# Kernel optimization log

Measured on AMD Instinct MI355X. Metric: run time of the kernel, lower is better.

## Reference

```python
import jax, jax.numpy as jnp
import numpy as np
from jax.scipy.special import logsumexp

S, B, T = 512, 1024, 48


def setup_inputs() -> dict:
    key = jax.random.key(0)
    k1, k2, k3, k4, k5 = jax.random.split(key, 5)
    return {
        "emissions": jax.random.normal(k1, (S, B, T), jnp.float32),
        "tags": jax.random.randint(k2, (S, B), 0, T, jnp.int32),
        "mask": jnp.ones((S, B), jnp.float32),
        "transitions": jax.random.normal(k3, (T, T), jnp.float32),
        "start_transitions": jax.random.normal(k4, (T,), jnp.float32),
        "stop_transitions": jax.random.normal(k5, (T,), jnp.float32),
    }


def _crf(emissions, tags, mask, transitions, start, stop):
    # emissions: (S,B,T), tags/mask: (S,B), time-major as in the torch module
    init = start[None, :] + emissions[0]  # (B,T)

    def step(carry, inp):
        fv, vv = carry  # forward (logsumexp) and viterbi (max) vars, each (B,T)
        em, m = inp  # (B,T), (B,)
        # scores[b, next, prev] = prev_var + transitions[prev,next] swapped to match
        # torch: forward_var.unsqueeze(1) + emission.unsqueeze(2) + transitions.unsqueeze(0)
        sc_f = fv[:, None, :] + transitions[None, :, :] + em[:, :, None]  # (B,T,T)
        sc_v = vv[:, None, :] + transitions[None, :, :] + em[:, :, None]
        new_fv = logsumexp(sc_f, axis=2)
        new_vv = jnp.max(sc_v, axis=2)
        m_ = m[:, None]
        fv = m_ * new_fv + (1.0 - m_) * fv
        vv = m_ * new_vv + (1.0 - m_) * vv
        return (fv, vv), None

    (fv, vv), _ = jax.lax.scan(step, (init, init), (emissions[1:], mask[1:]))
    alpha = logsumexp(fv + stop[None, :], axis=1)  # total_score (B,)
    best_path_score = jnp.max(vv + stop[None, :], axis=1)  # (B,)

    # real (gold) path score, fully vectorized over time
    em_tag = jnp.take_along_axis(emissions, tags[:, :, None].astype(jnp.int32), axis=2)[:, :, 0]  # (S,B)
    trans_sc = transitions[tags[:-1], tags[1:]]  # (S-1,B)
    real = (start[tags[0]]
            + jnp.sum(mask[1:] * (trans_sc + em_tag[1:]), axis=0)
            + stop[tags[-1]])
    loss = jnp.mean(alpha - real)
    return loss, real, alpha, best_path_score


def reference(emissions, tags, mask, transitions, start_transitions, stop_transitions):
    # Training-mode forward (return_best_path=False -> best_path is None in torch)
    return _crf(emissions, tags, mask, transitions, start_transitions, stop_transitions)
```

## Files before the change

kernel.cpp:

```cpp
#include <hip/hip_runtime.h>
#include <hip/hip_fp16.h>

#define S_LEN 512
#define B_DIM 1024
#define T_DIM 48
#define L2E 1.4426950408889634f
#define LN2 0.6931471805599453f

#define EXP2F(x) __builtin_amdgcn_exp2f(x)
#define LOG2F(x) __builtin_amdgcn_logf(x)

typedef _Float16 h2v __attribute__((ext_vector_type(2)));

__device__ __forceinline__ __half2 hmax2(__half2 a, __half2 b) {
  h2v r = __builtin_elementwise_max(__builtin_bit_cast(h2v, a),
                                    __builtin_bit_cast(h2v, b));
  return __builtin_bit_cast(__half2, r);
}

__device__ __forceinline__ __half2 bpick(__half2 src, int lane) {
  int s = __builtin_amdgcn_readlane(__builtin_bit_cast(int, src), lane);
  return __builtin_bit_cast(__half2, s);
}

template <int CTRL, int RMASK>
__device__ __forceinline__ float dppmovf(float v) {
  return __int_as_float(__builtin_amdgcn_update_dpp(
      __float_as_int(v), __float_as_int(v), CTRL, RMASK, 0xF, false));
}
template <int CTRL, int RMASK>
__device__ __forceinline__ float dppmaxf(float m) {
  return fmaxf(m, dppmovf<CTRL, RMASK>(m));
}
template <int CTRL, int RMASK>
__device__ __forceinline__ float dppaddf(float m) {
  return m + dppmovf<CTRL, RMASK>(m);
}

__device__ __forceinline__ float wave_max63(float m) {
  m = dppmaxf<0xB1, 0xF>(m);
  m = dppmaxf<0x4E, 0xF>(m);
  m = dppmaxf<0x141, 0xF>(m);
  m = dppmaxf<0x140, 0xF>(m);
  m = dppmaxf<0x142, 0xA>(m);
  m = dppmaxf<0x143, 0xC>(m);
  return __int_as_float(__builtin_amdgcn_readlane(__float_as_int(m), 63));
}
__device__ __forceinline__ float wave_sum63(float m) {
  m = dppaddf<0xB1, 0xF>(m);
  m = dppaddf<0x4E, 0xF>(m);
  m = dppaddf<0x141, 0xF>(m);
  m = dppaddf<0x140, 0xF>(m);
  m = dppaddf<0x142, 0xA>(m);
  m = dppaddf<0x143, 0xC>(m);
  return __int_as_float(__builtin_amdgcn_readlane(__float_as_int(m), 63));
}

__global__ __launch_bounds__(192, 3)
void crf_fused(const float* __restrict__ em, const int* __restrict__ tags,
               const float* __restrict__ mask, const float* __restrict__ trans,
               const float* __restrict__ startT, const float* __restrict__ stopT,
               float* __restrict__ out)
{
  const int b    = blockIdx.x;
  const int wave = threadIdx.x >> 6;
  const int i    = threadIdx.x & 63;

  if (wave == 2) {
    float acc = 0.f;
#pragma unroll
    for (int k = 0; k < 8; ++k) {
      int s = 1 + i + (k << 6);
      if (s < S_LEN) {
        int   tp  = tags[(s - 1) * B_DIM + b];
        int   tc  = tags[s * B_DIM + b];
        float mkv = mask[s * B_DIM + b];
        float emt = em[((size_t)s * B_DIM + b) * T_DIM + tc];
        acc = fmaf(mkv, trans[tp * T_DIM + tc] + emt, acc);
      }
    }
    float tot = wave_sum63(acc);
    if (i == 0)
      out[1 + b] = startT[tags[b]] + stopT[tags[(S_LEN - 1) * B_DIM + b]] + tot;
    return;
  }

  const int ri = (i < T_DIM) ? i : (T_DIM - 1);

  const float* emb = em + (size_t)b * T_DIM + ri;
  const size_t estep = (size_t)B_DIM * T_DIM;
  float e1 = emb[1 * estep], e2 = emb[2 * estep], e3 = emb[3 * estep];
  float e4 = emb[4 * estep], e5 = emb[5 * estep], e6 = emb[6 * estep];
  float mk1 = mask[1 * B_DIM + b], mk2 = mask[2 * B_DIM + b];
  float mk3 = mask[3 * B_DIM + b], mk4 = mask[4 * B_DIM + b];
  float mk5 = mask[5 * B_DIM + b], mk6 = mask[6 * B_DIM + b];
  const float* pf  = emb + 7 * estep;
  const float* pmk = mask + 7 * B_DIM + b;

#define SHIFT_REGS                                                   \
      e1 = e2; e2 = e3; e3 = e4; e4 = e5; e5 = e6; e6 = ep;          \
      mk1 = mk2; mk2 = mk3; mk3 = mk4; mk4 = mk5; mk5 = mk6; mk6 = mkp;

  if (wave == 0) {
#define DECL_E(n) __half2 E##n = __floats2half2_rn( \
      EXP2F(trans[ri * T_DIM + 2*(n)    ] * L2E),   \
      EXP2F(trans[ri * T_DIM + 2*(n) + 1] * L2E));
    DECL_E(0)  DECL_E(1)  DECL_E(2)  DECL_E(3)  DECL_E(4)  DECL_E(5)
    DECL_E(6)  DECL_E(7)  DECL_E(8)  DECL_E(9)  DECL_E(10) DECL_E(11)
    DECL_E(12) DECL_E(13) DECL_E(14) DECL_E(15) DECL_E(16) DECL_E(17)
    DECL_E(18) DECL_E(19) DECL_E(20) DECL_E(21) DECL_E(22) DECL_E(23)

#define PIN_E asm("" : "+v"(E0), "+v"(E1), "+v"(E2), "+v"(E3),       \
      "+v"(E4), "+v"(E5), "+v"(E6), "+v"(E7), "+v"(E8), "+v"(E9),    \
      "+v"(E10), "+v"(E11), "+v"(E12), "+v"(E13), "+v"(E14),         \
      "+v"(E15), "+v"(E16), "+v"(E17), "+v"(E18), "+v"(E19),         \
      "+v"(E20), "+v"(E21), "+v"(E22), "+v"(E23));

    float p  = EXP2F((startT[ri] + emb[0]) * L2E);
    float k2 = 0.f;

#define FVG(g, Ea, Eb, Ec, Ed, Ee, Ef)                 \
    { __half2 t0 = bpick(pp, 12*(g) + 0);              \
      __half2 t1 = bpick(pp, 12*(g) + 2);              \
      __half2 t2 = bpick(pp, 12*(g) + 4);              \
      __half2 t3 = bpick(pp, 12*(g) + 6);              \
      __half2 t4 = bpick(pp, 12*(g) + 8);              \
      __half2 t5 = bpick(pp, 12*(g) + 10);             \
      a0 = __hfma2(t0, Ea, a0);                        \
      a1 = __hfma2(t1, Eb, a1);                        \
      a2 = __hfma2(t2, Ec, a2);                        \
      a3 = __hfma2(t3, Ed, a3);                        \
      a0 = __hfma2(t4, Ee, a0);                        \
      a1 = __hfma2(t5, Ef, a1); }

#define FV_STEP(LOAD)                                                \
    { float ep, mkp;                                                 \
      if (LOAD) { ep = *pf; pf += estep; mkp = *pmk; pmk += B_DIM; } \
      else      { ep = e6; mkp = mk6; }                              \
      PIN_E                                                          \
      float pm = wave_max63(p);               \
      float lg = LOG2F(pm);                                          \
      float c  = EXP2F(-lg - 8.0f);                   \
      k2 += lg + 8.0f;                                               \
      float pn = dppmovf<0xB1, 0xF>(p);                              \
      __half2 pp = __floats2half2_rn(p, pn);                         \
      __half2 a0 = __float2half2_rn(0.f), a1 = a0, a2 = a0, a3 = a0; \
      FVG(0, E0,  E1,  E2,  E3,  E4,  E5)                            \
      FVG(1, E6,  E7,  E8,  E9,  E10, E11)                           \
      FVG(2, E12, E13, E14, E15, E16, E17)                           \
      FVG(3, E18, E19, E20, E21, E22, E23)                           \
      a0 = __hadd2(a0, a1); a2 = __hadd2(a2, a3); a0 = __hadd2(a0, a2); \
      float accF  = __low2float(a0) + __high2float(a0);              \
      float expem = EXP2F(e1 * L2E);                                 \
      float t  = accF * expem * c;                                   \
      float pc = p * c;                                              \
      p = fminf(fmaf(mk1, t - pc, pc), 1024.0f);                     \
      SHIFT_REGS }

#pragma unroll 6
    for (int s = 1; s <= 504; ++s) FV_STEP(true)
    FV_STEP(true)
    FV_STEP(false) FV_STEP(false) FV_STEP(false)
    FV_STEP(false) FV_STEP(false) FV_STEP(false)

    float q = p * EXP2F(stopT[ri] * L2E);
    q = (i < T_DIM) ? q : 0.f;
    float Sq = wave_sum63(q);
    float alpha = LN2 * (k2 + LOG2F(Sq));
    if (i == 0) out[1 + B_DIM + b] = alpha;
  } else {
#define DECL_T(n) __half2 T##n = __floats2half2_rn( \
      trans[ri * T_DIM + 2*(n)], trans[ri * T_DIM + 2*(n) + 1]);
    DECL_T(0)  DECL_T(1)  DECL_T(2)  DECL_T(3)  DECL_T(4)  DECL_T(5)
    DECL_T(6)  DECL_T(7)  DECL_T(8)  DECL_T(9)  DECL_T(10) DECL_T(11)
    DECL_T(12) DECL_T(13) DECL_T(14) DECL_T(15) DECL_T(16) DECL_T(17)
    DECL_T(18) DECL_T(19) DECL_T(20) DECL_T(21) DECL_T(22) DECL_T(23)

#define PIN_T asm("" : "+v"(T0), "+v"(T1), "+v"(T2), "+v"(T3),       \
      "+v"(T4), "+v"(T5), "+v"(T6), "+v"(T7), "+v"(T8), "+v"(T9),    \
      "+v"(T10), "+v"(T11), "+v"(T12), "+v"(T13), "+v"(T14),         \
      "+v"(T15), "+v"(T16), "+v"(T17), "+v"(T18), "+v"(T19),         \
      "+v"(T20), "+v"(T21), "+v"(T22), "+v"(T23));

    float v = startT[ri] + emb[0];
    const __half2 NEGI = __floats2half2_rn(-60000.f, -60000.f);
    float m_ref = wave_max63(v);

#define VVG(g, Ta, Tb, Tc, Td, Te, Tf)                 \
    { __half2 t0 = bpick(vp, 12*(g) + 0);              \
      __half2 t1 = bpick(vp, 12*(g) + 2);              \
      __half2 t2 = bpick(vp, 12*(g) + 4);              \
      __half2 t3 = bpick(vp, 12*(g) + 6);              \
      __half2 t4 = bpick(vp, 12*(g) + 8);              \
      __half2 t5 = bpick(vp, 12*(g) + 10);             \
      m0 = hmax2(m0, __hadd2(t0, Ta));                 \
      m1 = hmax2(m1, __hadd2(t1, Tb));                 \
      m2 = hmax2(m2, __hadd2(t2, Tc));                 \
      m3 = hmax2(m3, __hadd2(t3, Td));                 \
      m0 = hmax2(m0, __hadd2(t4, Te));                 \
      m1 = hmax2(m1, __hadd2(t5, Tf)); }

#define VV_STEP(LOAD, DOTREE)                                        \
    { float ep, mkp;                                                 \
      if (LOAD) { ep = *pf; pf += estep; mkp = *pmk; pmk += B_DIM; } \
      else      { ep = e6; mkp = mk6; }                              \
      PIN_T                                                          \
      if (DOTREE) m_ref = wave_max63(v);                             \
      float vr  = v - m_ref;                                         \
      float vn_ = dppmovf<0xB1, 0xF>(vr);                            \
      __half2 vp = __floats2half2_rn(vr, vn_);                       \
      __half2 m0 = NEGI, m1 = NEGI, m2 = NEGI, m3 = NEGI;            \
      VVG(0, T0,  T1,  T2,  T3,  T4,  T5)                            \
      VVG(1, T6,  T7,  T8,  T9,  T10, T11)                           \
      VVG(2, T12, T13, T14, T15, T16, T17)                           \
      VVG(3, T18, T19, T20, T21, T22, T23)                           \
      m0 = hmax2(hmax2(m0, m1), hmax2(m2, m3));                      \
      float mx = fmaxf(__low2float(m0), __high2float(m0));           \
      float vnew = e1 + m_ref + mx;                                  \
      v = fmaf(mk1, vnew - v, v);                                    \
      SHIFT_REGS }

#pragma unroll 8
    for (int s = 1; s <= 504; ++s) VV_STEP(true, ((s & 7) == 0))
    VV_STEP(true, false)
    VV_STEP(false, false) VV_STEP(false, false) VV_STEP(false, false)
    VV_STEP(false, false) VV_STEP(false, false) VV_STEP(false, false)

    float best = wave_max63(v + stopT[ri]);
    if (i == 0) out[1 + 2 * B_DIM + b] = best;
  }
}

__global__ __launch_bounds__(256)
void crf_loss(float* __restrict__ out)
{
  __shared__ float red[256];
  int t = threadIdx.x;
  float a = 0.f;
  for (int b = t; b < B_DIM; b += 256)
    a += out[1 + B_DIM + b] - out[1 + b];
  red[t] = a;
  __syncthreads();
  for (int w = 128; w > 0; w >>= 1) {
    if (t < w) red[t] += red[t + w];
    __syncthreads();
  }
  if (t == 0) out[0] = red[0] * (1.0f / B_DIM);
}

extern "C" void kernel_launch(void* const* d_in, const int* in_sizes, int n_in,
                              void* d_out, int out_size, void* d_ws, size_t ws_size,
                              hipStream_t stream) {
  (void)in_sizes; (void)n_in; (void)d_ws; (void)ws_size; (void)out_size;
  const float* em     = (const float*)d_in[0];
  const int*   tags   = (const int*)d_in[1];
  const float* mask   = (const float*)d_in[2];
  const float* trans  = (const float*)d_in[3];
  const float* startT = (const float*)d_in[4];
  const float* stopT  = (const float*)d_in[5];
  float* out = (float*)d_out;

  hipLaunchKernelGGL(crf_fused, dim3(B_DIM), dim3(192), 0, stream,
                     em, tags, mask, trans, startT, stopT, out);
  hipLaunchKernelGGL(crf_loss, dim3(1), dim3(256), 0, stream, out);
}
```

Before: 201.5 us.

## Lockstep waves with periodic barriers and replace log/exp rescale with exponent bit tricks

Restructures the forward and Viterbi time loops into 63 groups of 8 steps, with a workgroup barrier after each group. The gold-path wave joins the same barriers, so the three waves stay in lockstep and their loads and issue slots may interleave better. The per-step log2/exp2 rescale in the forward wave is replaced by reading the float exponent bits and building a power-of-two scale factor. The per-step register pin asm becomes a single volatile pin before each loop. Barriers add stall points if the waves run at different speeds, and dropping the per-step pin may let the compiler spill or reload the transition registers.

```diff
diff --git a/kernel.cpp b/kernel.cpp
--- a/kernel.cpp
+++ b/kernel.cpp
@@ -68,16 +68,18 @@
 
   if (wave == 2) {
     float acc = 0.f;
-#pragma unroll
-    for (int k = 0; k < 8; ++k) {
-      int s = 1 + i + (k << 6);
-      if (s < S_LEN) {
-        int   tp  = tags[(s - 1) * B_DIM + b];
-        int   tc  = tags[s * B_DIM + b];
-        float mkv = mask[s * B_DIM + b];
-        float emt = em[((size_t)s * B_DIM + b) * T_DIM + tc];
-        acc = fmaf(mkv, trans[tp * T_DIM + tc] + emt, acc);
+    for (int g = 0; g < 63; ++g) {
+      if (g < 8) {
+        int s = 1 + i + (g << 6);
+        if (s < S_LEN) {
+          int   tp  = tags[(s - 1) * B_DIM + b];
+          int   tc  = tags[s * B_DIM + b];
+          float mkv = mask[s * B_DIM + b];
+          float emt = em[((size_t)s * B_DIM + b) * T_DIM + tc];
+          acc = fmaf(mkv, trans[tp * T_DIM + tc] + emt, acc);
+        }
       }
+      __builtin_amdgcn_s_barrier();
     }
     float tot = wave_sum63(acc);
     if (i == 0)
@@ -110,10 +112,10 @@
     DECL_E(12) DECL_E(13) DECL_E(14) DECL_E(15) DECL_E(16) DECL_E(17)
     DECL_E(18) DECL_E(19) DECL_E(20) DECL_E(21) DECL_E(22) DECL_E(23)
 
-#define PIN_E asm("" : "+v"(E0), "+v"(E1), "+v"(E2), "+v"(E3),       \
-      "+v"(E4), "+v"(E5), "+v"(E6), "+v"(E7), "+v"(E8), "+v"(E9),    \
-      "+v"(E10), "+v"(E11), "+v"(E12), "+v"(E13), "+v"(E14),         \
-      "+v"(E15), "+v"(E16), "+v"(E17), "+v"(E18), "+v"(E19),         \
+    asm volatile("" : "+v"(E0), "+v"(E1), "+v"(E2), "+v"(E3),
+      "+v"(E4), "+v"(E5), "+v"(E6), "+v"(E7), "+v"(E8), "+v"(E9),
+      "+v"(E10), "+v"(E11), "+v"(E12), "+v"(E13), "+v"(E14),
+      "+v"(E15), "+v"(E16), "+v"(E17), "+v"(E18), "+v"(E19),
       "+v"(E20), "+v"(E21), "+v"(E22), "+v"(E23));
 
     float p  = EXP2F((startT[ri] + emb[0]) * L2E);
@@ -137,11 +139,10 @@
     { float ep, mkp;                                                 \
       if (LOAD) { ep = *pf; pf += estep; mkp = *pmk; pmk += B_DIM; } \
       else      { ep = e6; mkp = mk6; }                              \
-      PIN_E                                                          \
-      float pm = wave_max63(p);               \
-      float lg = LOG2F(pm);                                          \
-      float c  = EXP2F(-lg - 8.0f);                   \
-      k2 += lg + 8.0f;                                               \
+      float pm = wave_max63(p);                                      \
+      int ee   = (__float_as_int(pm) >> 23) - 126;    \
+      float c  = __int_as_float((127 - ee) << 23);  \
+      k2 += (float)ee;                                               \
       float pn = dppmovf<0xB1, 0xF>(p);                              \
       __half2 pp = __floats2half2_rn(p, pn);                         \
       __half2 a0 = __float2half2_rn(0.f), a1 = a0, a2 = a0, a3 = a0; \
@@ -157,8 +158,11 @@
       p = fminf(fmaf(mk1, t - pc, pc), 1024.0f);                     \
       SHIFT_REGS }
 
-#pragma unroll 6
-    for (int s = 1; s <= 504; ++s) FV_STEP(true)
+    for (int g = 0; g < 63; ++g) {
+#pragma unroll
+      for (int u = 0; u < 8; ++u) FV_STEP(true)
+      __builtin_amdgcn_s_barrier();
+    }
     FV_STEP(true)
     FV_STEP(false) FV_STEP(false) FV_STEP(false)
     FV_STEP(false) FV_STEP(false) FV_STEP(false)
@@ -176,10 +180,10 @@
     DECL_T(12) DECL_T(13) DECL_T(14) DECL_T(15) DECL_T(16) DECL_T(17)
     DECL_T(18) DECL_T(19) DECL_T(20) DECL_T(21) DECL_T(22) DECL_T(23)
 
-#define PIN_T asm("" : "+v"(T0), "+v"(T1), "+v"(T2), "+v"(T3),       \
-      "+v"(T4), "+v"(T5), "+v"(T6), "+v"(T7), "+v"(T8), "+v"(T9),    \
-      "+v"(T10), "+v"(T11), "+v"(T12), "+v"(T13), "+v"(T14),         \
-      "+v"(T15), "+v"(T16), "+v"(T17), "+v"(T18), "+v"(T19),         \
+    asm volatile("" : "+v"(T0), "+v"(T1), "+v"(T2), "+v"(T3),
+      "+v"(T4), "+v"(T5), "+v"(T6), "+v"(T7), "+v"(T8), "+v"(T9),
+      "+v"(T10), "+v"(T11), "+v"(T12), "+v"(T13), "+v"(T14),
+      "+v"(T15), "+v"(T16), "+v"(T17), "+v"(T18), "+v"(T19),
       "+v"(T20), "+v"(T21), "+v"(T22), "+v"(T23));
 
     float v = startT[ri] + emb[0];
@@ -204,7 +208,6 @@
     { float ep, mkp;                                                 \
       if (LOAD) { ep = *pf; pf += estep; mkp = *pmk; pmk += B_DIM; } \
       else      { ep = e6; mkp = mk6; }                              \
-      PIN_T                                                          \
       if (DOTREE) m_ref = wave_max63(v);                             \
       float vr  = v - m_ref;                                         \
       float vn_ = dppmovf<0xB1, 0xF>(vr);                            \
@@ -220,8 +223,12 @@
       v = fmaf(mk1, vnew - v, v);                                    \
       SHIFT_REGS }
 
-#pragma unroll 8
-    for (int s = 1; s <= 504; ++s) VV_STEP(true, ((s & 7) == 0))
+    for (int g = 0; g < 63; ++g) {
+#pragma unroll
+      for (int u = 0; u < 7; ++u) VV_STEP(true, false)
+      VV_STEP(true, true)
+      __builtin_amdgcn_s_barrier();
+    }
     VV_STEP(true, false)
     VV_STEP(false, false) VV_STEP(false, false) VV_STEP(false, false)
     VV_STEP(false, false) VV_STEP(false, false) VV_STEP(false, false)
```

Result: slower. 208.7 us (+3.5%).
